# Kernel optimization log

Measured on AMD Instinct MI355X. Metric: run time of the kernel, lower is better.

## Reference

```python
import jax, jax.numpy as jnp
import numpy as np

N, B = 1024, 32
PEP_PAD, L, M, E, VOCAB = 3, 27, 34, 16, 26
CN, KS, OFFS = (128, 256, 256), (3, 5, 7), (2, 1, 0)
LIN = (512, 256)
BN_EPS = 1e-5


def _pe(length, d):
    pos = np.arange(length, dtype=np.float32)[:, None]
    div = np.exp(np.arange(0, d, 2, dtype=np.float32) * (-np.log(10000.0) / d))
    pe = np.zeros((length, d), np.float32)
    pe[:, 0::2] = np.sin(pos * div)
    pe[:, 1::2] = np.cos(pos * div)
    return jnp.asarray(pe)

PE_MHC = _pe(M, E)
PE_PEP = _pe(100, E)[: L - 2 * PEP_PAD]


def _bn(x, g, b):
    # inference-mode BatchNorm2d (running_mean=0, running_var=1)
    s = g / jnp.sqrt(1.0 + BN_EPS)
    return x * s[None, :, None, None] + b[None, :, None, None]


def _iconv(pep, mhc, W, b):
    # interaction conv: pep (N, Lin, E, S), mhc (N, M, E), W (C, K, M)
    # out[n,c,i,s] = sum_{k,m,e} W[c,k,m] * mhc[n,m,e] * pep[n,i+k,e,s] + b[c]
    K = W.shape[1]
    Kb = jnp.einsum('ckm,nme->ncke', W, mhc)  # per-sample kernel (N,C,K,E)
    Lout = pep.shape[1] - K + 1
    out = sum(jnp.einsum('nce,nies->ncis', Kb[:, :, k], pep[:, k:k + Lout]) for k in range(K))
    return out + b[None, :, None, None]


def _fwd(params, peptide_x, mhc_x, bags_size, inverse):
    (emb_pep, emb_mhc, convs_f, convs_r, lins_f, lins_r,
     w_att1, b_att1, w_att2, b_att2, w_out, b_out) = params
    masks = peptide_x[:, PEP_PAD:L - PEP_PAD] != 0              # (N, 21)
    mhc_e = emb_mhc[mhc_x] + PE_MHC                             # (N, 34, E)
    pep_e = emb_pep[peptide_x]
    pep_e = jnp.concatenate([pep_e[:, :PEP_PAD],
                             pep_e[:, PEP_PAD:L - PEP_PAD] + PE_PEP,
                             pep_e[:, L - PEP_PAD:]], axis=1)    # (N, 27, E)
    pep_c = pep_e[..., None]                                     # (N,27,E,1)
    pep_i = jnp.stack([pep_e[:, ::-1], pep_e], axis=-1)          # (N,27,E,2)

    def branch(pep, convs, inversion):
        outs = []
        for (W, bb, g, be), off in zip(convs, OFFS):
            Wk = W[:, ::-1] if inversion else W
            x = _iconv(pep[:, off:L - off], mhc_e, Wk, bb)
            outs.append(jax.nn.relu(_bn(x, g, be)))
        return jnp.concatenate(outs, axis=1)

    conv_out = branch(pep_c, convs_f, False)                     # (N, 640, 21, 1)
    conv_r = branch(pep_i, convs_r, True)                        # (N, 640, 21, 2)
    conv_r = jnp.concatenate([conv_r[..., 0:1][:, :, ::-1], conv_r[..., 1:2]], axis=-1)

    def mlp(x, lins):
        for Wl, bl, gl, bel in lins:
            x = jax.nn.relu(_bn(jnp.einsum('oc,nciw->noiw', Wl, x) + bl[None, :, None, None], gl, bel))
        return x

    conv_out = mlp(conv_out, lins_f)                             # (N, 256, 21, 1)
    conv_r = mlp(conv_r, lins_r)                                 # (N, 256, 21, 2)
    x = jnp.concatenate([conv_out, conv_r], axis=-1)             # (N, 256, 21, 3)
    m = masks[:, None, -x.shape[2]:, None]
    pool = jnp.max(jnp.where(m, x, -jnp.inf), axis=2, keepdims=True)  # (N,256,1,3)

    # attention MIL over variable-size bags (segment softmax)
    feat = pool.mean(axis=(2, 3))                                # (N, 256)
    a = (jnp.tanh(feat @ w_att1.T + b_att1) @ w_att2.T + b_att2)[:, 0]
    nb = bags_size.shape[0]
    seg = jnp.repeat(jnp.arange(nb), bags_size, total_repeat_length=feat.shape[0])
    amax = jax.lax.stop_gradient(jax.ops.segment_max(a, seg, num_segments=nb))
    ex = jnp.exp(a - amax[seg])
    att = ex / jax.ops.segment_sum(ex, seg, num_segments=nb)[seg]

    score = jax.nn.sigmoid(jnp.einsum('oc,nciw->noiw', w_out, pool) + b_out[None, :, None, None])  # (N,2,1,3)
    half = score[..., :2].sum(-1) * 0.5
    if inverse:
        s = jnp.stack([half, score[..., -1]], axis=-1)           # (N,2,1,2)
    else:
        s = jnp.stack([half, half], axis=-1)
    s = s.max(axis=-1)                                           # (N, 2, 1)
    if inverse:
        s = jax.ops.segment_sum(att[:, None, None] * s, seg, num_segments=nb)  # (B,2,1)
    else:
        s = s.sum(axis=-1) * 0.5
    s = jnp.clip(s, 0.0, 1.0)
    return s.reshape(s.shape[0], -1)                             # (B, 2)


def setup_inputs() -> dict:
    key = jax.random.key(0)
    ks = iter(jax.random.split(key, 64))
    nrm = lambda shape, std=0.02: jax.random.normal(next(ks), shape, jnp.float32) * std
    d = {}
    d['peptide_x'] = jax.random.randint(next(ks), (N, L), 1, VOCAB)
    d['mhc_x'] = jax.random.randint(next(ks), (N, M), 1, VOCAB)
    d['context_x'] = jax.random.randint(next(ks), (N, 12), 1, VOCAB)
    d['peptide_esm_x'] = jnp.zeros((N, 2, 10, 3), jnp.float32)
    d['bags_size'] = jnp.full((B,), N // B, jnp.int32)
    d['inverse'] = 1
    d['emb_pep'] = jax.random.uniform(next(ks), (VOCAB, E), jnp.float32, -0.1, 0.1)
    d['emb_mhc'] = jax.random.uniform(next(ks), (VOCAB, E), jnp.float32, -0.1, 0.1)
    for tag in ('cf', 'cr'):
        for j, (c, k) in enumerate(zip(CN, KS)):
            d[f'w_{tag}{j}'] = nrm((c, k, M), 0.05)
            d[f'b_{tag}{j}'] = jnp.zeros((c,), jnp.float32)
            d[f'g_{tag}{j}'] = 1.0 + nrm((c,), 0.002)
            d[f'be_{tag}{j}'] = jnp.zeros((c,), jnp.float32)
    dims = [sum(CN)] + list(LIN)
    for tag in ('lf', 'lr'):
        for j, (i_s, o_s) in enumerate(zip(dims[:-1], dims[1:])):
            d[f'w_{tag}{j}'] = nrm((o_s, i_s), 0.02)
            d[f'b_{tag}{j}'] = jnp.zeros((o_s,), jnp.float32)
            d[f'g_{tag}{j}'] = 1.0 + nrm((o_s,), 0.002)
            d[f'be_{tag}{j}'] = jnp.zeros((o_s,), jnp.float32)
    H = LIN[-1]
    d['w_att1'] = nrm((H, H)); d['b_att1'] = jnp.zeros((H,), jnp.float32)
    d['w_att2'] = nrm((1, H)); d['b_att2'] = jnp.zeros((1,), jnp.float32)
    d['w_out'] = nrm((2, H), 0.1); d['b_out'] = jnp.zeros((2,), jnp.float32)
    return d


def reference(peptide_x, mhc_x, context_x, peptide_esm_x, bags_size, inverse,
              emb_pep, emb_mhc,
              w_cf0, b_cf0, g_cf0, be_cf0, w_cf1, b_cf1, g_cf1, be_cf1, w_cf2, b_cf2, g_cf2, be_cf2,
              w_cr0, b_cr0, g_cr0, be_cr0, w_cr1, b_cr1, g_cr1, be_cr1, w_cr2, b_cr2, g_cr2, be_cr2,
              w_lf0, b_lf0, g_lf0, be_lf0, w_lf1, b_lf1, g_lf1, be_lf1,
              w_lr0, b_lr0, g_lr0, be_lr0, w_lr1, b_lr1, g_lr1, be_lr1,
              w_att1, b_att1, w_att2, b_att2, w_out, b_out):
    convs_f = [(w_cf0, b_cf0, g_cf0, be_cf0), (w_cf1, b_cf1, g_cf1, be_cf1), (w_cf2, b_cf2, g_cf2, be_cf2)]
    convs_r = [(w_cr0, b_cr0, g_cr0, be_cr0), (w_cr1, b_cr1, g_cr1, be_cr1), (w_cr2, b_cr2, g_cr2, be_cr2)]
    lins_f = [(w_lf0, b_lf0, g_lf0, be_lf0), (w_lf1, b_lf1, g_lf1, be_lf1)]
    lins_r = [(w_lr0, b_lr0, g_lr0, be_lr0), (w_lr1, b_lr1, g_lr1, be_lr1)]
    params = (emb_pep, emb_mhc, convs_f, convs_r, lins_f, lins_r,
              w_att1, b_att1, w_att2, b_att2, w_out, b_out)
    return _fwd(params, peptide_x, mhc_x, bags_size, int(inverse))
```

## Files before the change

### kernel.cpp

```cpp
#include <hip/hip_runtime.h>
#include <hip/hip_bf16.h>
#include <math.h>

#define NS   1024
#define LP   27
#define MMH  34
#define EE   16
#define LO   21
#define CT   640
#define H1   512
#define H2   256
#define LPAD 40
#define GROW (LP*LPAD)
#define SLOTROWS (NS*LO)
#define ALLROWS  (3*SLOTROWS)

typedef __attribute__((ext_vector_type(8))) short  s8v;
typedef __attribute__((ext_vector_type(4))) float  f4v;

#define PK2_SLOT 147456
#define PK2_J0   0
#define PK2_J1   16384
#define PK2_J2   73728
#define WMLP_FAM 458752
#define WMLP_B   327680
#define BMLP_FAM 768
#define BMLP_B   512

__device__ __forceinline__ ushort f2b(float v) {
    __hip_bfloat16 hb = __float2bfloat16(v);
    return *reinterpret_cast<ushort*>(&hb);
}

__device__ __forceinline__ float pe_val(int pos, int e) {
    int j = e >> 1;
    float div = expf(-1.1512925464970229f * (float)j);
    float ang = (float)pos * div;
    return (e & 1) ? cosf(ang) : sinf(ang);
}

__device__ __forceinline__ int xcd_swz() {
    int fid = blockIdx.y * gridDim.x + blockIdx.x;
    int nwg = gridDim.x * gridDim.y;
    int cpx = nwg >> 3;
    return (fid & 7) * cpx + (fid >> 3);
}

struct PrepArgs {
    const int* pep_x; const int* mhc_x;
    const float* emb_pep; const float* emb_mhc;
    const float* cw[2][3]; const float* cb[2][3]; const float* cg[2][3]; const float* cbe[2][3];
    const float* mw[4]; const float* mb[4]; const float* mg[4]; const float* mbe[4];
    ushort* Gb; ushort* Wpack; float* bpack; ushort* Wmlp; float* bmlp; int* poolI;
};

__global__ __launch_bounds__(256) void k_prep(PrepArgs A) {
    int b = blockIdx.x, t = threadIdx.x;
    float rs = rsqrtf(1.0f + 1e-5f);
    if (b < NS) {
        __shared__ float ps[LP * 17];
        __shared__ float ms[MMH * 17];
        int n = b;
        for (int idx = t; idx < LP * EE; idx += 256) {
            int l = idx >> 4, e = idx & 15;
            float v = A.emb_pep[A.pep_x[n * LP + l] * EE + e];
            if (l >= 3 && l < 24) v += pe_val(l - 3, e);
            ps[l * 17 + e] = v;
        }
        for (int idx = t; idx < MMH * EE; idx += 256) {
            int m = idx >> 4, e = idx & 15;
            ms[m * 17 + e] = A.emb_mhc[A.mhc_x[n * MMH + m] * EE + e] + pe_val(m, e);
        }
        __syncthreads();
        for (int idx = t; idx < GROW; idx += 256) {
            int l = idx / LPAD, m = idx - l * LPAD;
            float s = 0.f;
            if (m < MMH) {
                #pragma unroll
                for (int e = 0; e < EE; ++e) s = fmaf(ps[l * 17 + e], ms[m * 17 + e], s);
            }
            A.Gb[(size_t)n * GROW + idx] = f2b(s);
        }
        if (n == 0 && t < 64) A.Gb[(size_t)NS * GROW + t] = 0;
    } else if (b < NS + 144) {
        const int KS_[3]  = {3, 5, 7};
        const int KCP_[3] = {128, 224, 288};
        const int NC_[3]  = {128, 256, 256};
        const int pkoff[3] = {PK2_J0, PK2_J1, PK2_J2};
        const int bpoff[3] = {0, 128, 384};
        int lin = b - NS;
        int s = lin / 48, rem = lin - s * 48, j = rem >> 4, z = rem & 15;
        int K = KS_[j], Kcp = KCP_[j], nc = NC_[j];
        int fam = (s == 0) ? 0 : 1;
        const float* w  = A.cw[fam][j];
        const float* g  = A.cg[fam][j];
        ushort* Wp = A.Wpack + s * PK2_SLOT + pkoff[j];
        int tot = nc * Kcp;
        for (int idx = z * 256 + t; idx < tot; idx += 16 * 256) {
            int c = idx / Kcp, col = idx - c * Kcp;
            int k = col / LPAD, m = col - k * LPAD;
            float v = 0.f;
            if (k < K && m < MMH) {
                int kk = (s == 2) ? (K - 1 - k) : k;
                v = w[((size_t)c * K + kk) * MMH + m] * (g[c] * rs);
            }
            Wp[idx] = f2b(v);
        }
        if (z == 0) {
            const float* bb = A.cb[fam][j];
            const float* be = A.cbe[fam][j];
            float* bp = A.bpack + s * CT + bpoff[j];
            for (int c = t; c < nc; c += 256)
                bp[c] = bb[c] * (g[c] * rs) + be[c];
        }
    } else if (b < NS + 144 + 112) {
        int lin = b - NS - 144;
        int task, rel, nb;
        if (lin < 40)      { task = 0; rel = lin;      nb = 40; }
        else if (lin < 56) { task = 1; rel = lin - 40; nb = 16; }
        else if (lin < 96) { task = 2; rel = lin - 56; nb = 40; }
        else               { task = 3; rel = lin - 96; nb = 16; }
        int fam = task >> 1, stage = task & 1;
        int Co = stage ? H2 : H1;
        int Ci = stage ? H1 : CT;
        const float* w  = A.mw[task];
        const float* g  = A.mg[task];
        ushort* Wb = A.Wmlp + fam * WMLP_FAM + stage * WMLP_B;
        int tot = Co * Ci;
        for (int idx = rel * 256 + t; idx < tot; idx += nb * 256) {
            int o = idx / Ci;
            Wb[idx] = f2b(w[idx] * (g[o] * rs));
        }
        if (rel == 0) {
            const float* bb = A.mb[task];
            const float* be = A.mbe[task];
            float* bp = A.bmlp + fam * BMLP_FAM + stage * BMLP_B;
            for (int o = t; o < Co; o += 256)
                bp[o] = bb[o] * (g[o] * rs) + be[o];
        }
    } else {
        int base = (b - NS - 144 - 112) * 8192;
        #pragma unroll
        for (int q = 0; q < 32; ++q)
            A.poolI[base + q * 256 + t] = 0;
    }
}

__global__ __launch_bounds__(256) void k_cmfma(
    const ushort* __restrict__ Gb, const ushort* __restrict__ Wpack,
    const float* __restrict__ bpack, ushort* __restrict__ Xb, int rowBase)
{
    const int kcpm[5] = {128, 224, 224, 288, 288};
    const int offm[5] = {2, 1, 1, 0, 0};
    const int o0m[5]  = {0, 0, 128, 0, 128};
    const int c0m[5]  = {0, 128, 128, 384, 384};
    const int wofm[5] = {PK2_J0, PK2_J1, PK2_J1, PK2_J2, PK2_J2};

    __shared__ ushort smC[17408];
    ushort* Al = smC;
    ushort* Bl = smC + 5120;
    int wg = xcd_swz();
    int y = wg % 5, rtile = wg / 5;
    int Kcp = kcpm[y], off = offm[y], o0 = o0m[y];
    int c0X = c0m[y] + o0;
    int r0g = rowBase + rtile * 128;
    int slot = r0g / SLOTROWS;
    const ushort* Wt = Wpack + slot * PK2_SLOT + wofm[y] + (size_t)o0 * Kcp;
    const float*  bp = bpack + slot * CT;
    int p0 = rtile * 128;

    int t = threadIdx.x, lane = t & 63, w = t >> 6;
    int r0 = (w >> 1) * 64, c0w = (w & 1) * 64;

    int row_a = t >> 2, seg = t & 3;
    int rg0 = r0g + row_a, rg1 = rg0 + 64;
    int rr0 = rg0 - slot * SLOTROWS, rr1 = rg1 - slot * SLOTROWS;
    size_t wb0 = (size_t)(rr0 / LO) * GROW + (off + rr0 % LO) * LPAD;
    size_t wb1 = (size_t)(rr1 / LO) * GROW + (off + rr1 % LO) * LPAD;

    f4v acc[4][4];
    #pragma unroll
    for (int m = 0; m < 4; ++m)
        #pragma unroll
        for (int n = 0; n < 4; ++n)
            acc[m][n] = (f4v){0.f, 0.f, 0.f, 0.f};

    int nkt = Kcp >> 5;
    for (int kt = 0; kt < nkt; ++kt) {
        int k0 = kt << 5;
        __syncthreads();
        *(s8v*)&Al[row_a * 40 + seg * 8]        = *(const s8v*)&Gb[wb0 + k0 + seg * 8];
        *(s8v*)&Al[(row_a + 64) * 40 + seg * 8] = *(const s8v*)&Gb[wb1 + k0 + seg * 8];
        *(s8v*)&Bl[row_a * 40 + seg * 8]        = *(const s8v*)&Wt[(size_t)row_a * Kcp + k0 + seg * 8];
        *(s8v*)&Bl[(row_a + 64) * 40 + seg * 8] = *(const s8v*)&Wt[(size_t)(row_a + 64) * Kcp + k0 + seg * 8];
        __syncthreads();
        s8v a[4], b[4];
        #pragma unroll
        for (int m = 0; m < 4; ++m)
            a[m] = *(const s8v*)&Al[(r0 + m * 16 + (lane & 15)) * 40 + (lane >> 4) * 8];
        #pragma unroll
        for (int n = 0; n < 4; ++n)
            b[n] = *(const s8v*)&Bl[(c0w + n * 16 + (lane & 15)) * 40 + (lane >> 4) * 8];
        #pragma unroll
        for (int m = 0; m < 4; ++m)
            #pragma unroll
            for (int n = 0; n < 4; ++n)
                acc[m][n] = __builtin_amdgcn_mfma_f32_16x16x32_bf16(a[m], b[n], acc[m][n], 0, 0, 0);
    }

    int cl = lane & 15, rq = lane >> 4;
    __syncthreads();
    #pragma unroll
    for (int m = 0; m < 4; ++m)
        #pragma unroll
        for (int n = 0; n < 4; ++n) {
            int ocr = c0w + n * 16 + cl;
            float bv = bp[c0X + ocr];
            #pragma unroll
            for (int j = 0; j < 4; ++j)
                smC[(r0 + m * 16 + rq * 4 + j) * 136 + ocr] = f2b(fmaxf(acc[m][n][j] + bv, 0.f));
        }
    __syncthreads();
    int ci = t & 15;
    #pragma unroll
    for (int it = 0; it < 8; ++it) {
        int row = (t >> 4) + it * 16;
        *(s8v*)&Xb[(size_t)(p0 + row) * CT + c0X + ci * 8] = *(const s8v*)&smC[row * 136 + ci * 8];
    }
}

__global__ __launch_bounds__(256) void k_mgemmA(
    const ushort* __restrict__ Xin,
    const ushort* __restrict__ Wbase, const float* __restrict__ bbase,
    ushort* __restrict__ Yb, int rowBase)
{
    __shared__ ushort smA[18432];
    ushort* Al = smA;
    ushort* Bl = smA + 9216;
    int t = threadIdx.x;
    int wg = xcd_swz();
    int o0 = (wg & 3) * 128;
    int p0 = (wg >> 2) * 128;
    int g0 = rowBase + p0;
    int fam = (g0 < SLOTROWS) ? 0 : 1;
    const ushort* Wb = Wbase + (size_t)fam * WMLP_FAM;
    const float*  bp = bbase + fam * BMLP_FAM;
    int lane = t & 63, w = t >> 6;
    int r0 = (w >> 1) * 64, c0 = (w & 1) * 64;

    f4v acc[4][4];
    #pragma unroll
    for (int m = 0; m < 4; ++m)
        #pragma unroll
        for (int n = 0; n < 4; ++n)
            acc[m][n] = (f4v){0.f, 0.f, 0.f, 0.f};

    for (int kt = 0; kt < CT / 64; ++kt) {
        int k0 = kt << 6;
        __syncthreads();
        #pragma unroll
        for (int it = 0; it < 4; ++it) {
            int idx = t + it * 256;
            int row = idx >> 3, sg = idx & 7;
            *(s8v*)&Al[row * 72 + sg * 8] = *(const s8v*)&Xin[(size_t)(p0 + row) * CT + k0 + sg * 8];
            *(s8v*)&Bl[row * 72 + sg * 8] = *(const s8v*)&Wb[(size_t)(o0 + row) * CT + k0 + sg * 8];
        }
        __syncthreads();
        #pragma unroll
        for (int ks = 0; ks < 2; ++ks) {
            int kc = ks * 32 + (lane >> 4) * 8;
            s8v a[4], b[4];
            #pragma unroll
            for (int m = 0; m < 4; ++m)
                a[m] = *(const s8v*)&Al[(r0 + m * 16 + (lane & 15)) * 72 + kc];
            #pragma unroll
            for (int n = 0; n < 4; ++n)
                b[n] = *(const s8v*)&Bl[(c0 + n * 16 + (lane & 15)) * 72 + kc];
            #pragma unroll
            for (int m = 0; m < 4; ++m)
                #pragma unroll
                for (int n = 0; n < 4; ++n)
                    acc[m][n] = __builtin_amdgcn_mfma_f32_16x16x32_bf16(a[m], b[n], acc[m][n], 0, 0, 0);
        }
    }

    int cl = lane & 15, rq = lane >> 4;
    __syncthreads();
    #pragma unroll
    for (int m = 0; m < 4; ++m)
        #pragma unroll
        for (int n = 0; n < 4; ++n) {
            int ocr = c0 + n * 16 + cl;
            float bv = bp[o0 + ocr];
            #pragma unroll
            for (int j = 0; j < 4; ++j)
                smA[(r0 + m * 16 + rq * 4 + j) * 136 + ocr] = f2b(fmaxf(acc[m][n][j] + bv, 0.f));
        }
    __syncthreads();
    int ci = t & 15;
    #pragma unroll
    for (int it = 0; it < 8; ++it) {
        int row = (t >> 4) + it * 16;
        *(s8v*)&Yb[(size_t)(p0 + row) * H1 + o0 + ci * 8] = *(const s8v*)&smA[row * 136 + ci * 8];
    }
}

__global__ __launch_bounds__(256) void k_mgemmB(
    const ushort* __restrict__ Yin,
    const ushort* __restrict__ Wbase, const float* __restrict__ bbase,
    const int* __restrict__ pep_x, int* __restrict__ poolI, int rowBase)
{
    __shared__ float zbuf[128 * 129];
    __shared__ int mvalid[128];
    ushort* Al = (ushort*)zbuf;
    ushort* Bl = Al + 9216;
    int t = threadIdx.x;
    int wg = xcd_swz();
    int o0 = (wg & 1) * 128;
    int p0 = (wg >> 1) * 128;
    int g0 = rowBase + p0;
    int slot = g0 / SLOTROWS;
    int gs0 = g0 - slot * SLOTROWS;
    int fam = (slot == 0) ? 0 : 1;
    const ushort* Wb = Wbase + (size_t)fam * WMLP_FAM + WMLP_B;
    const float*  bp = bbase + fam * BMLP_FAM + BMLP_B;
    int lane = t & 63, w = t >> 6;
    int r0 = (w >> 1) * 64, c0 = (w & 1) * 64;

    f4v acc[4][4];
    #pragma unroll
    for (int m = 0; m < 4; ++m)
        #pragma unroll
        for (int n = 0; n < 4; ++n)
            acc[m][n] = (f4v){0.f, 0.f, 0.f, 0.f};

    for (int kt = 0; kt < H1 / 64; ++kt) {
        int k0 = kt << 6;
        __syncthreads();
        #pragma unroll
        for (int it = 0; it < 4; ++it) {
            int idx = t + it * 256;
            int row = idx >> 3, sg = idx & 7;
            *(s8v*)&Al[row * 72 + sg * 8] = *(const s8v*)&Yin[(size_t)(p0 + row) * H1 + k0 + sg * 8];
            *(s8v*)&Bl[row * 72 + sg * 8] = *(const s8v*)&Wb[(size_t)(o0 + row) * H1 + k0 + sg * 8];
        }
        __syncthreads();
        #pragma unroll
        for (int ks = 0; ks < 2; ++ks) {
            int kc = ks * 32 + (lane >> 4) * 8;
            s8v a[4], b[4];
            #pragma unroll
            for (int m = 0; m < 4; ++m)
                a[m] = *(const s8v*)&Al[(r0 + m * 16 + (lane & 15)) * 72 + kc];
            #pragma unroll
            for (int n = 0; n < 4; ++n)
                b[n] = *(const s8v*)&Bl[(c0 + n * 16 + (lane & 15)) * 72 + kc];
            #pragma unroll
            for (int m = 0; m < 4; ++m)
                #pragma unroll
                for (int n = 0; n < 4; ++n)
                    acc[m][n] = __builtin_amdgcn_mfma_f32_16x16x32_bf16(a[m], b[n], acc[m][n], 0, 0, 0);
        }
    }

    int cl = lane & 15, rq = lane >> 4;
    __syncthreads();
    if (t < 128) {
        int gs = gs0 + t;
        int n = gs / LO, i = gs - n * LO;
        mvalid[t] = (pep_x[n * LP + 3 + i] != 0) ? 1 : 0;
    }
    #pragma unroll
    for (int m = 0; m < 4; ++m)
        #pragma unroll
        for (int n = 0; n < 4; ++n) {
            int ocr = c0 + n * 16 + cl;
            float bv = bp[o0 + ocr];
            #pragma unroll
            for (int j = 0; j < 4; ++j)
                zbuf[(r0 + m * 16 + rq * 4 + j) * 129 + ocr] = fmaxf(acc[m][n][j] + bv, 0.f);
        }
    __syncthreads();

    int col = t & 127, half = t >> 7;
    int colg = o0 + col;
    int rs = half * 64;
    int gs = gs0 + rs;
    int n = gs / LO, i = gs - n * LO;
    float cur = -1.f;
    for (int r = rs; r < rs + 64; ++r) {
        if (mvalid[r]) cur = fmaxf(cur, zbuf[r * 129 + col]);
        if (++i == LO) {
            if (cur >= 0.f)
                atomicMax(&poolI[n * (3 * H2) + slot * H2 + colg], __float_as_int(cur));
            cur = -1.f; ++n; i = 0;
        }
    }
    if (cur >= 0.f)
        atomicMax(&poolI[n * (3 * H2) + slot * H2 + colg], __float_as_int(cur));
}

__global__ __launch_bounds__(256) void k_poolhead(
    const float* __restrict__ pool,
    const float* __restrict__ w_att1, const float* __restrict__ b_att1,
    const float* __restrict__ w_att2, const float* __restrict__ b_att2,
    const float* __restrict__ w_out, const float* __restrict__ b_out,
    float* __restrict__ a_out, float* __restrict__ s2_out)
{
    int n = blockIdx.x, c = threadIdx.x;
    __shared__ float feat_s[H2];
    __shared__ float red[7][H2];
    __shared__ float sc_s[6];

    float mx[3];
    #pragma unroll
    for (int w = 0; w < 3; ++w)
        mx[w] = pool[(size_t)n * (3 * H2) + w * H2 + c];

    float fv = (mx[0] + mx[1] + mx[2]) * (1.f / 3.f);
    feat_s[c] = fv;
    #pragma unroll
    for (int o = 0; o < 2; ++o)
        #pragma unroll
        for (int w = 0; w < 3; ++w)
            red[o * 3 + w][c] = w_out[o * H2 + c] * mx[w];
    __syncthreads();

    float hacc = 0.f;
    for (int cc = 0; cc < H2; ++cc)
        hacc = fmaf(w_att1[(size_t)c * H2 + cc], feat_s[cc], hacc);
    float h = tanhf(hacc + b_att1[c]);
    red[6][c] = h * w_att2[c];
    __syncthreads();

    for (int s = 128; s > 0; s >>= 1) {
        if (c < s) {
            #pragma unroll
            for (int jj = 0; jj < 7; ++jj) red[jj][c] += red[jj][c + s];
        }
        __syncthreads();
    }
    if (c == 0) a_out[n] = red[6][0] + b_att2[0];
    if (c < 6) {
        float x = red[c][0] + b_out[c / 3];
        sc_s[c] = 1.f / (1.f + expf(-x));
    }
    __syncthreads();
    if (c < 2) {
        float half = 0.5f * (sc_s[c * 3 + 0] + sc_s[c * 3 + 1]);
        s2_out[n * 2 + c] = fmaxf(half, sc_s[c * 3 + 2]);
    }
}

__global__ __launch_bounds__(1024) void k_final(
    const float* __restrict__ a_in, const float* __restrict__ s2_in,
    const int* __restrict__ bags, float* __restrict__ out)
{
    __shared__ float a_s[NS], s0_s[NS], s1_s[NS];
    __shared__ int off_s[33];
    int t = threadIdx.x;
    a_s[t]  = a_in[t];
    s0_s[t] = s2_in[t * 2 + 0];
    s1_s[t] = s2_in[t * 2 + 1];
    if (t == 0) {
        off_s[0] = 0;
        for (int g = 0; g < 32; ++g) off_s[g + 1] = off_s[g] + bags[g];
    }
    __syncthreads();
    if (t < 32) {
        int st = off_s[t], en = off_s[t + 1];
        float mxv = -INFINITY;
        for (int n = st; n < en; ++n) mxv = fmaxf(mxv, a_s[n]);
        float se = 0.f;
        for (int n = st; n < en; ++n) se += expf(a_s[n] - mxv);
        float inv = 1.f / se;
        float o0 = 0.f, o1 = 0.f;
        for (int n = st; n < en; ++n) {
            float w = expf(a_s[n] - mxv) * inv;
            o0 += w * s0_s[n];
            o1 += w * s1_s[n];
        }
        out[t * 2 + 0] = fminf(fmaxf(o0, 0.f), 1.f);
        out[t * 2 + 1] = fminf(fmaxf(o1, 0.f), 1.f);
    }
}

extern "C" void kernel_launch(void* const* d_in, const int* in_sizes, int n_in,
                              void* d_out, int out_size, void* d_ws, size_t ws_size,
                              hipStream_t stream) {
    const int* pep_x = (const int*)d_in[0];
    const int* mhc_x = (const int*)d_in[1];
    const int* bags  = (const int*)d_in[4];

    char* wsb = (char*)d_ws;
    float*  pool   = (float*) (wsb + 0);
    int*    poolI  = (int*)   (wsb + 0);
    float*  a_buf  = (float*) (wsb + 3145728);
    float*  s2_buf = (float*) (wsb + 3149824);
    ushort* Wpack  = (ushort*)(wsb + 3158016);
    float*  bpack  = (float*) (wsb + 4042752);
    ushort* Wmlp   = (ushort*)(wsb + 4050432);
    float*  bmlp   = (float*) (wsb + 5885440);
    ushort* Gb     = (ushort*)(wsb + 5891584);
    const size_t XB_B = 8103552;

    size_t fullNeed = XB_B + (size_t)ALLROWS * (1280 + 1024);
    int chunkSlots = (fullNeed <= ws_size) ? 3 : 1;
    int RC = chunkSlots * SLOTROWS;
    ushort* Xb = (ushort*)(wsb + XB_B);
    ushort* Yb = (ushort*)((char*)Xb + (size_t)RC * 1280);

    PrepArgs pa;
    pa.pep_x = pep_x; pa.mhc_x = mhc_x;
    pa.emb_pep = (const float*)d_in[6];
    pa.emb_mhc = (const float*)d_in[7];
    for (int j = 0; j < 3; ++j) {
        pa.cw[0][j]  = (const float*)d_in[8 + 4 * j];
        pa.cb[0][j]  = (const float*)d_in[9 + 4 * j];
        pa.cg[0][j]  = (const float*)d_in[10 + 4 * j];
        pa.cbe[0][j] = (const float*)d_in[11 + 4 * j];
        pa.cw[1][j]  = (const float*)d_in[20 + 4 * j];
        pa.cb[1][j]  = (const float*)d_in[21 + 4 * j];
        pa.cg[1][j]  = (const float*)d_in[22 + 4 * j];
        pa.cbe[1][j] = (const float*)d_in[23 + 4 * j];
    }
    for (int task = 0; task < 4; ++task) {
        int base = 32 + task * 4;
        pa.mw[task]  = (const float*)d_in[base + 0];
        pa.mb[task]  = (const float*)d_in[base + 1];
        pa.mg[task]  = (const float*)d_in[base + 2];
        pa.mbe[task] = (const float*)d_in[base + 3];
    }
    pa.Gb = Gb; pa.Wpack = Wpack; pa.bpack = bpack; pa.Wmlp = Wmlp; pa.bmlp = bmlp;
    pa.poolI = poolI;

    k_prep<<<dim3(NS + 144 + 112 + 96), dim3(256), 0, stream>>>(pa);

    for (int rowBase = 0; rowBase < ALLROWS; rowBase += RC) {
        int nRB = RC / 128;
        k_cmfma<<<dim3(5, nRB), dim3(256), 0, stream>>>(Gb, Wpack, bpack, Xb, rowBase);
        k_mgemmA<<<dim3(H1 / 128, nRB), dim3(256), 0, stream>>>(Xb, Wmlp, bmlp, Yb, rowBase);
        k_mgemmB<<<dim3(H2 / 128, nRB), dim3(256), 0, stream>>>(Yb, Wmlp, bmlp, pep_x, poolI, rowBase);
    }

    k_poolhead<<<dim3(NS), dim3(256), 0, stream>>>(
        pool,
        (const float*)d_in[48], (const float*)d_in[49], (const float*)d_in[50], (const float*)d_in[51],
        (const float*)d_in[52], (const float*)d_in[53],
        a_buf, s2_buf);

    k_final<<<dim3(1), dim3(1024), 0, stream>>>(a_buf, s2_buf, bags, (float*)d_out);
}
```

Before: 194.9 us.

## Use direct global-to-LDS loads with k-chunk-major LDS layout in GEMM kernels

Replaces the register-staged global-load-then-LDS-store tile fills in the conv MFMA kernel and both MLP GEMMs with global_load_lds 16-byte transfers straight into shared memory. The LDS tiles are rearranged from padded row-major into k-chunk-major blocks of 8 elements per row, so each wave's contiguous write lands where the MFMA fragment reads expect it. This is meant to cut VGPR traffic and instruction count on the load path. In exchange the padding that avoided bank conflicts is gone, and correctness now depends on the builtin's per-wave LDS addressing matching the chosen layout.

```diff
diff --git a/kernel.cpp b/kernel.cpp
--- a/kernel.cpp
+++ b/kernel.cpp
@@ -37,6 +37,12 @@
     float div = expf(-1.1512925464970229f * (float)j);
     float ang = (float)pos * div;
     return (e & 1) ? cosf(ang) : sinf(ang);
+}
+
+__device__ __forceinline__ void gl16(const ushort* g, ushort* l) {
+    __builtin_amdgcn_global_load_lds(
+        (const __attribute__((address_space(1))) void*)g,
+        (__attribute__((address_space(3))) void*)l, 16, 0, 0);
 }
 
 __device__ __forceinline__ int xcd_swz() {
@@ -158,7 +164,7 @@
 
     __shared__ ushort smC[17408];
     ushort* Al = smC;
-    ushort* Bl = smC + 5120;
+    ushort* Bl = smC + 4096;
     int wg = xcd_swz();
     int y = wg % 5, rtile = wg / 5;
     int Kcp = kcpm[y], off = offm[y], o0 = o0m[y];
@@ -169,14 +175,17 @@
     const float*  bp = bpack + slot * CT;
     int p0 = rtile * 128;
 
-    int t = threadIdx.x, lane = t & 63, w = t >> 6;
-    int r0 = (w >> 1) * 64, c0w = (w & 1) * 64;
-
-    int row_a = t >> 2, seg = t & 3;
-    int rg0 = r0g + row_a, rg1 = rg0 + 64;
-    int rr0 = rg0 - slot * SLOTROWS, rr1 = rg1 - slot * SLOTROWS;
-    size_t wb0 = (size_t)(rr0 / LO) * GROW + (off + rr0 % LO) * LPAD;
-    size_t wb1 = (size_t)(rr1 / LO) * GROW + (off + rr1 % LO) * LPAD;
+    int t = threadIdx.x, lane = t & 63, wv = t >> 6;
+    int r0 = (wv >> 1) * 64, c0w = (wv & 1) * 64;
+
+    int rowL = t & 127;
+    int kbT  = t >> 7;
+    int rgl = r0g + rowL;
+    int rrl = rgl - slot * SLOTROWS;
+    const ushort* srcA = Gb + (size_t)(rrl / LO) * GROW + (off + rrl % LO) * LPAD + kbT * 8;
+    const ushort* srcB = Wt + (size_t)rowL * Kcp + kbT * 8;
+    int d0 = wv * 512;
+    int d1 = 2048 + wv * 512;
 
     f4v acc[4][4];
     #pragma unroll
@@ -189,18 +198,19 @@
     for (int kt = 0; kt < nkt; ++kt) {
         int k0 = kt << 5;
         __syncthreads();
-        *(s8v*)&Al[row_a * 40 + seg * 8]        = *(const s8v*)&Gb[wb0 + k0 + seg * 8];
-        *(s8v*)&Al[(row_a + 64) * 40 + seg * 8] = *(const s8v*)&Gb[wb1 + k0 + seg * 8];
-        *(s8v*)&Bl[row_a * 40 + seg * 8]        = *(const s8v*)&Wt[(size_t)row_a * Kcp + k0 + seg * 8];
-        *(s8v*)&Bl[(row_a + 64) * 40 + seg * 8] = *(const s8v*)&Wt[(size_t)(row_a + 64) * Kcp + k0 + seg * 8];
+        gl16(srcA + k0,      &Al[d0]);
+        gl16(srcA + k0 + 16, &Al[d1]);
+        gl16(srcB + k0,      &Bl[d0]);
+        gl16(srcB + k0 + 16, &Bl[d1]);
         __syncthreads();
         s8v a[4], b[4];
+        int kq = (lane >> 4) * 1024;
         #pragma unroll
         for (int m = 0; m < 4; ++m)
-            a[m] = *(const s8v*)&Al[(r0 + m * 16 + (lane & 15)) * 40 + (lane >> 4) * 8];
+            a[m] = *(const s8v*)&Al[kq + (r0 + m * 16 + (lane & 15)) * 8];
         #pragma unroll
         for (int n = 0; n < 4; ++n)
-            b[n] = *(const s8v*)&Bl[(c0w + n * 16 + (lane & 15)) * 40 + (lane >> 4) * 8];
+            b[n] = *(const s8v*)&Bl[kq + (c0w + n * 16 + (lane & 15)) * 8];
         #pragma unroll
         for (int m = 0; m < 4; ++m)
             #pragma unroll
@@ -234,9 +244,9 @@
     const ushort* __restrict__ Wbase, const float* __restrict__ bbase,
     ushort* __restrict__ Yb, int rowBase)
 {
-    __shared__ ushort smA[18432];
+    __shared__ ushort smA[17408];
     ushort* Al = smA;
-    ushort* Bl = smA + 9216;
+    ushort* Bl = smA + 8192;
     int t = threadIdx.x;
     int wg = xcd_swz();
     int o0 = (wg & 3) * 128;
@@ -245,8 +255,14 @@
     int fam = (g0 < SLOTROWS) ? 0 : 1;
     const ushort* Wb = Wbase + (size_t)fam * WMLP_FAM;
     const float*  bp = bbase + fam * BMLP_FAM;
-    int lane = t & 63, w = t >> 6;
-    int r0 = (w >> 1) * 64, c0 = (w & 1) * 64;
+    int lane = t & 63, wv = t >> 6;
+    int r0 = (wv >> 1) * 64, c0 = (wv & 1) * 64;
+
+    int rowL = t & 127;
+    int kbT  = t >> 7;
+    const ushort* srcA = Xin + (size_t)(p0 + rowL) * CT + kbT * 8;
+    const ushort* srcB = Wb + (size_t)(o0 + rowL) * CT + kbT * 8;
+    int dw = wv * 512;
 
     f4v acc[4][4];
     #pragma unroll
@@ -260,22 +276,20 @@
         __syncthreads();
         #pragma unroll
         for (int it = 0; it < 4; ++it) {
-            int idx = t + it * 256;
-            int row = idx >> 3, sg = idx & 7;
-            *(s8v*)&Al[row * 72 + sg * 8] = *(const s8v*)&Xin[(size_t)(p0 + row) * CT + k0 + sg * 8];
-            *(s8v*)&Bl[row * 72 + sg * 8] = *(const s8v*)&Wb[(size_t)(o0 + row) * CT + k0 + sg * 8];
+            gl16(srcA + k0 + it * 16, &Al[it * 2048 + dw]);
+            gl16(srcB + k0 + it * 16, &Bl[it * 2048 + dw]);
         }
         __syncthreads();
         #pragma unroll
         for (int ks = 0; ks < 2; ++ks) {
-            int kc = ks * 32 + (lane >> 4) * 8;
+            int kq = (ks * 4 + (lane >> 4)) * 1024;
             s8v a[4], b[4];
             #pragma unroll
             for (int m = 0; m < 4; ++m)
-                a[m] = *(const s8v*)&Al[(r0 + m * 16 + (lane & 15)) * 72 + kc];
+                a[m] = *(const s8v*)&Al[kq + (r0 + m * 16 + (lane & 15)) * 8];
             #pragma unroll
             for (int n = 0; n < 4; ++n)
-                b[n] = *(const s8v*)&Bl[(c0 + n * 16 + (lane & 15)) * 72 + kc];
+                b[n] = *(const s8v*)&Bl[kq + (c0 + n * 16 + (lane & 15)) * 8];
             #pragma unroll
             for (int m = 0; m < 4; ++m)
                 #pragma unroll
@@ -313,7 +327,7 @@
     __shared__ float zbuf[128 * 129];
     __shared__ int mvalid[128];
     ushort* Al = (ushort*)zbuf;
-    ushort* Bl = Al + 9216;
+    ushort* Bl = Al + 8192;
     int t = threadIdx.x;
     int wg = xcd_swz();
     int o0 = (wg & 1) * 128;
@@ -324,8 +338,14 @@
     int fam = (slot == 0) ? 0 : 1;
     const ushort* Wb = Wbase + (size_t)fam * WMLP_FAM + WMLP_B;
     const float*  bp = bbase + fam * BMLP_FAM + BMLP_B;
-    int lane = t & 63, w = t >> 6;
-    int r0 = (w >> 1) * 64, c0 = (w & 1) * 64;
+    int lane = t & 63, wv = t >> 6;
+    int r0 = (wv >> 1) * 64, c0 = (wv & 1) * 64;
+
+    int rowL = t & 127;
+    int kbT  = t >> 7;
+    const ushort* srcA = Yin + (size_t)(p0 + rowL) * H1 + kbT * 8;
+    const ushort* srcB = Wb + (size_t)(o0 + rowL) * H1 + kbT * 8;
+    int dw = wv * 512;
 
     f4v acc[4][4];
     #pragma unroll
@@ -339,22 +359,20 @@
         __syncthreads();
         #pragma unroll
         for (int it = 0; it < 4; ++it) {
-            int idx = t + it * 256;
-            int row = idx >> 3, sg = idx & 7;
-            *(s8v*)&Al[row * 72 + sg * 8] = *(const s8v*)&Yin[(size_t)(p0 + row) * H1 + k0 + sg * 8];
-            *(s8v*)&Bl[row * 72 + sg * 8] = *(const s8v*)&Wb[(size_t)(o0 + row) * H1 + k0 + sg * 8];
+            gl16(srcA + k0 + it * 16, &Al[it * 2048 + dw]);
+            gl16(srcB + k0 + it * 16, &Bl[it * 2048 + dw]);
         }
         __syncthreads();
         #pragma unroll
         for (int ks = 0; ks < 2; ++ks) {
-            int kc = ks * 32 + (lane >> 4) * 8;
+            int kq = (ks * 4 + (lane >> 4)) * 1024;
             s8v a[4], b[4];
             #pragma unroll
             for (int m = 0; m < 4; ++m)
-                a[m] = *(const s8v*)&Al[(r0 + m * 16 + (lane & 15)) * 72 + kc];
+                a[m] = *(const s8v*)&Al[kq + (r0 + m * 16 + (lane & 15)) * 8];
             #pragma unroll
             for (int n = 0; n < 4; ++n)
-                b[n] = *(const s8v*)&Bl[(c0 + n * 16 + (lane & 15)) * 72 + kc];
+                b[n] = *(const s8v*)&Bl[kq + (c0 + n * 16 + (lane & 15)) * 8];
             #pragma unroll
             for (int m = 0; m < 4; ++m)
                 #pragma unroll
```

After: 255.3 us. 1.31x slower.
